# Performance work log

Measured on AMD Instinct MI355X. Metric: run time of the kernel, lower is better.

## Reference

```python
import jax, jax.numpy as jnp
import numpy as np

N = 16384      # tokens
D_IN = 256     # input feature dim
D = 1024       # d_model
H = 2048       # expert hidden dim (2 * d_model)
E = 8          # n_experts
K = 2          # top_k
OUT = 2        # output classes
EPS = 1e-5


def layernorm(x, g, b):
    m = jnp.mean(x, axis=-1, keepdims=True)
    v = jnp.mean(jnp.square(x - m), axis=-1, keepdims=True)
    return (x - m) * jax.lax.rsqrt(v + EPS) * g + b


def setup_inputs() -> dict:
    key = jax.random.key(0)
    ks = jax.random.split(key, 10)
    s_in = 1.0 / np.sqrt(D_IN)
    s_d = 1.0 / np.sqrt(D)
    s_h = 1.0 / np.sqrt(H)
    return {
        "x": jax.random.normal(ks[0], (N, D_IN), jnp.float32),
        "w_in": jax.random.normal(ks[1], (D_IN, D), jnp.float32) * s_in,
        "b_in": jnp.zeros((D,), jnp.float32),
        "g_in": jnp.ones((D,), jnp.float32),
        "beta_in": jnp.zeros((D,), jnp.float32),
        "w_gate": jax.random.normal(ks[2], (D, E), jnp.float32) * s_d,
        "w1": jax.random.normal(ks[3], (E, D, H), jnp.float32) * s_d,
        "b1": jnp.zeros((E, H), jnp.float32),
        "w2": jax.random.normal(ks[4], (E, H, D), jnp.float32) * s_h,
        "b2": jnp.zeros((E, D), jnp.float32),
        "g_moe": jnp.ones((D,), jnp.float32),
        "beta_moe": jnp.zeros((D,), jnp.float32),
        "g_out": jnp.ones((D,), jnp.float32),
        "beta_out": jnp.zeros((D,), jnp.float32),
        "w_cls": jax.random.normal(ks[5], (D, OUT), jnp.float32) * s_d,
        "b_cls": jnp.zeros((OUT,), jnp.float32),
    }


def reference(x, w_in, b_in, g_in, beta_in, w_gate, w1, b1, w2, b2,
              g_moe, beta_moe, g_out, beta_out, w_cls, b_cls):
    # input projection + norm
    h = layernorm(x @ w_in + b_in, g_in, beta_in)            # [N, D]
    # router: softmax then top-k, renormalize over selected experts
    probs = jax.nn.softmax(h @ w_gate, axis=-1)              # [N, E]
    _, top_idx = jax.lax.top_k(probs, K)                     # [N, K]
    sel = jax.nn.one_hot(top_idx, E, dtype=probs.dtype).sum(axis=1)  # [N, E] 0/1
    gates = probs * sel
    gates = gates / (jnp.sum(gates, axis=-1, keepdims=True) + 1e-9)
    # experts: weighted combine; gate==0 tokens contribute nothing (same math
    # as the torch masked gather/scatter-add, dropout off in eval)
    mixed = jnp.zeros_like(h)
    for e in range(E):  # fixed, small expert count
        expert_out = jax.nn.gelu(h @ w1[e] + b1[e]) @ w2[e] + b2[e]  # [N, D]
        mixed = mixed + gates[:, e:e + 1] * expert_out
    out = layernorm(h + mixed, g_moe, beta_moe)
    out = layernorm(out, g_out, beta_out)
    return out @ w_cls + b_cls                               # [N, OUT]
```

## Files before the change

kernel.cpp:

```cpp
#include <hip/hip_runtime.h>
#include <hip/hip_bf16.h>

#define D_IN 256
#define DM   1024
#define HD   2048
#define NE   8
#define NTOK 16384

typedef __attribute__((ext_vector_type(8))) short short8;
typedef __attribute__((ext_vector_type(4))) float f32x4;
typedef unsigned int uint;

#define MT_TOFF1 0
#define MT_TOFF2 512
#define MT_CNT1  1536
#define MT_P1    1600
#define MT_OFF1  1664
#define MT_CNT2  1728
#define MT_PCNT2 1856
#define MT_TOTAL 1984

__device__ inline ushort f2bf(float v){
  __hip_bfloat16 b = __float2bfloat16(v);
  return *reinterpret_cast<ushort*>(&b);
}
__device__ inline float bf2f(ushort u){
  __hip_bfloat16 b = *reinterpret_cast<__hip_bfloat16*>(&u);
  return __bfloat162float(b);
}

__device__ inline float gelu_fast(float x){
  float u = 0.7978845608028654f * x * (1.0f + 0.044715f*x*x);
  return x / (1.0f + __expf(-2.0f*u));
}

__device__ inline void gload16(const void* g, void* l){
  __builtin_amdgcn_global_load_lds(
      (const __attribute__((address_space(1))) void*)g,
      (__attribute__((address_space(3))) void*)l, 16, 0, 0);
}


__global__ __launch_bounds__(256) void transpose_both_kernel(
    const float* __restrict__ w1, const float* __restrict__ w2,
    ushort* __restrict__ w1t, ushort* __restrict__ w2t)
{
  __shared__ float tile[32][33];
  int bid = blockIdx.x;
  int which = bid >> 14;
  int r = bid & 16383;
  const float* src; ushort* dst; int R, C;
  if (which==0){ src=w1; dst=w1t; R=DM; C=HD; }
  else         { src=w2; dst=w2t; R=HD; C=DM; }
  int nbx = C/32, nby = R/32;
  int e = r / (nbx*nby); int rem = r % (nbx*nby);
  int c0 = (rem % nbx)*32, r0 = (rem / nbx)*32;
  src += (size_t)e*R*C; dst += (size_t)e*R*C;
  int tx = threadIdx.x & 31, ty = threadIdx.x >> 5;
  #pragma unroll
  for (int rr = ty; rr < 32; rr += 8)
    tile[rr][tx] = src[(size_t)(r0+rr)*C + c0+tx];
  __syncthreads();
  #pragma unroll
  for (int rr = ty; rr < 32; rr += 8)
    dst[(size_t)(c0+rr)*R + r0+tx] = f2bf(tile[tx][rr]);
}

__global__ __launch_bounds__(256) void split_x_kernel(
    const float* __restrict__ x, ushort* __restrict__ xs3)
{
  int g = blockIdx.x*256 + threadIdx.x;
  int e0 = g*4;
  int row = e0 >> 8, col = e0 & 255;
  f32x4 v = *(const f32x4*)(x + (size_t)row*D_IN + col);
  ushort4 hi, mi, lo;
  #pragma unroll
  for (int i=0;i<4;++i){
    float f = v[i];
    ushort h = f2bf(f);       float fh = bf2f(h);
    ushort m = f2bf(f - fh);  float fm = bf2f(m);
    ushort l = f2bf(f - fh - fm);
    ((ushort*)&hi)[i]=h; ((ushort*)&mi)[i]=m; ((ushort*)&lo)[i]=l;
  }
  ushort* base = xs3 + (size_t)row*768 + col;
  *(ushort4*)(base)       = hi;
  *(ushort4*)(base + 256) = mi;
  *(ushort4*)(base + 512) = lo;
}

__global__ __launch_bounds__(256) void transpose_split3_kernel(
    const float* __restrict__ src, ushort* __restrict__ dst)
{
  __shared__ float tile[32][33];
  int c0 = blockIdx.x*32, r0 = blockIdx.y*32;
  int tx = threadIdx.x & 31, ty = threadIdx.x >> 5;
  #pragma unroll
  for (int rr = ty; rr < 32; rr += 8)
    tile[rr][tx] = src[(size_t)(r0+rr)*DM + c0+tx];
  __syncthreads();
  #pragma unroll
  for (int rr = ty; rr < 32; rr += 8){
    float f = tile[tx][rr];
    ushort h = f2bf(f);       float fh = bf2f(h);
    ushort m = f2bf(f - fh);  float fm = bf2f(m);
    ushort l = f2bf(f - fh - fm);
    ushort* d = dst + (size_t)(c0+rr)*768 + r0 + tx;
    d[0]   = h;
    d[256] = m;
    d[512] = l;
  }
}

__global__ __launch_bounds__(256) void wgate_t_kernel(
    const float* __restrict__ w_gate, float* __restrict__ wgt)
{
  int e = blockIdx.x;
  for (int j = threadIdx.x; j < DM; j += 256)
    wgt[(size_t)e*DM + j] = w_gate[(size_t)j*NE + e];
}

__global__ __launch_bounds__(256) void gemm_router(
    const ushort* __restrict__ A,
    const ushort* __restrict__ BT,
    const float* __restrict__ b_in,
    float* __restrict__ y)
{
  __shared__ ushort As[3][128*32];
  __shared__ ushort Bs[3][128*32];
  const int tid = threadIdx.x;
  const int w = tid>>6, l = tid&63;
  const int wm = w>>1, wn = w&1;
  const int bm0 = blockIdx.y*128, bn0 = blockIdx.x*128;
  const int lr = l&15, lk = l>>4;
  const int rsub = l>>2;
  const int csub = ((l&3) ^ ((l>>3)&3)) * 8;

  const ushort* ag[2]; const ushort* bg[2];
  int aslot[2];
  #pragma unroll
  for (int i=0;i<2;++i){
    int ra = bm0 + w*32 + i*16 + rsub;
    int rb = bn0 + w*32 + i*16 + rsub;
    ag[i] = A  + (size_t)ra*768 + csub;
    bg[i] = BT + (size_t)rb*768 + csub;
    aslot[i] = (w*32 + i*16)*32;
  }

  const int pOffT[6] = {0,256,0,256,512,0};
  const int qOffT[6] = {0,0,256,256,0,512};
  auto stage = [&](int db, int t){
    int pOff = pOffT[t>>3] + (t&7)*32;
    int qOff = qOffT[t>>3] + (t&7)*32;
    #pragma unroll
    for (int i=0;i<2;++i){
      gload16(ag[i]+pOff, (ushort*)As[db] + aslot[i]);
      gload16(bg[i]+qOff, (ushort*)Bs[db] + aslot[i]);
    }
  };

  f32x4 acc[4][4] = {};
  const int NK = 48;
  stage(0, 0); stage(1, 1);
  int cur = 0;
  for (int t=0; t<NK; ++t){
    int sb = cur - 1; if (sb < 0) sb = 2;
    if (t+2 < NK)     { stage(sb, t+2); asm volatile("s_waitcnt vmcnt(8)" ::: "memory"); }
    else if (t+1 < NK){                 asm volatile("s_waitcnt vmcnt(4)" ::: "memory"); }
    else              {                 asm volatile("s_waitcnt vmcnt(0)" ::: "memory"); }
    __builtin_amdgcn_s_barrier();
    short8 af[4], bf[4];
    #pragma unroll
    for (int i=0;i<4;++i)
      af[i] = *(const short8*)(As[cur] + (wm*64 + i*16 + lr)*32 + (lk ^ ((lr>>1)&3))*8);
    #pragma unroll
    for (int j=0;j<4;++j)
      bf[j] = *(const short8*)(Bs[cur] + (wn*64 + j*16 + lr)*32 + (lk ^ ((lr>>1)&3))*8);
    __builtin_amdgcn_s_setprio(1);
    #pragma unroll
    for (int i=0;i<4;++i){
      #pragma unroll
      for (int j=0;j<4;++j)
        acc[i][j] = __builtin_amdgcn_mfma_f32_16x16x32_bf16(af[i], bf[j], acc[i][j], 0, 0, 0);
    }
    __builtin_amdgcn_s_setprio(0);
    __builtin_amdgcn_s_barrier();
    cur = cur + 1; if (cur > 2) cur = 0;
  }

  #pragma unroll
  for (int i=0;i<4;++i){
    #pragma unroll
    for (int j=0;j<4;++j){
      int n = bn0 + wn*64 + j*16 + lr;
      float bn_ = b_in[n];
      #pragma unroll
      for (int r=0;r<4;++r){
        int m = bm0 + wm*64 + i*16 + lk*4 + r;
        y[(size_t)m*DM + n] = acc[i][j][r] + bn_;
      }
    }
  }
}

__device__ inline double wredd(double v){
  #pragma unroll
  for (int o=32;o>0;o>>=1) v += __shfl_xor(v, o, 64);
  return v;
}

__global__ __launch_bounds__(256) void ln_router_kernel(
    const float* __restrict__ g_in, const float* __restrict__ beta_in,
    const float* __restrict__ wgt,
    ushort* __restrict__ hbf, float* __restrict__ resid,
    float* __restrict__ gates, int* __restrict__ selmask)
{
  int tok = blockIdx.x*4 + (threadIdx.x>>6);
  int l = threadIdx.x & 63;
  float* row = resid + (size_t)tok*DM;
  float u[16];
  double s=0.0, q=0.0;
  #pragma unroll
  for (int r=0;r<16;++r){ u[r]=row[l+64*r]; s+=u[r]; q+=(double)u[r]*u[r]; }
  s = wredd(s); q = wredd(q);
  double mean = s*(1.0/1024.0);
  double var  = q*(1.0/1024.0) - mean*mean;
  double rstd = 1.0/sqrt(var + 1e-5);

  double lg[NE];
  #pragma unroll
  for (int e=0;e<NE;++e) lg[e]=0.0;
  float hv[16];
  #pragma unroll
  for (int r=0;r<16;++r){
    int j = l + 64*r;
    double v = ((double)u[r]-mean)*rstd*(double)g_in[j] + (double)beta_in[j];
    hv[r] = (float)v;
    #pragma unroll
    for (int e=0;e<NE;++e) lg[e] += v*(double)wgt[(size_t)e*DM + j];
  }
  #pragma unroll
  for (int r=0;r<16;++r){
    int j = l + 64*r;
    row[j] = hv[r];
    hbf[(size_t)tok*DM + j] = f2bf(hv[r]);
  }
  #pragma unroll
  for (int e=0;e<NE;++e) lg[e] = wredd(lg[e]);

  if (l==0){
    double mx = lg[0];
    #pragma unroll
    for (int e=1;e<NE;++e) mx = lg[e]>mx ? lg[e] : mx;
    double p[NE]; double sum=0.0;
    #pragma unroll
    for (int e=0;e<NE;++e){ p[e]=exp(lg[e]-mx); sum+=p[e]; }
    #pragma unroll
    for (int e=0;e<NE;++e) p[e]/=sum;
    int i1=0;
    for (int e=1;e<NE;++e) if (p[e]>p[i1]) i1=e;
    int i2=-1;
    for (int e=0;e<NE;++e){ if (e==i1) continue; if (i2<0 || p[e]>p[i2]) i2=e; }
    double denom = p[i1]+p[i2]+1e-9;
    float g[NE];
    #pragma unroll
    for (int e=0;e<NE;++e) g[e]=0.f;
    g[i1]=(float)(p[i1]/denom);
    g[i2]=(float)(p[i2]/denom);
    #pragma unroll
    for (int e=0;e<NE;++e) gates[(size_t)tok*NE+e]=g[e];
    selmask[tok] = (1<<i1)|(1<<i2);
  }
}

__global__ __launch_bounds__(256) void builder_count(
    const int* __restrict__ selmask, uint* __restrict__ bc1, uint* __restrict__ bc2)
{
  __shared__ uint c1[8], c2s[16];
  int b = blockIdx.x, tid = threadIdx.x;
  if (tid<8) c1[tid]=0;
  if (tid<16) c2s[tid]=0;
  __syncthreads();
  int m = selmask[b*256+tid];
  int ea = __ffs(m)-1, eb = 31-__clz(m);
  atomicAdd(&c1[ea],1u); atomicAdd(&c1[eb],1u);
  atomicAdd(&c2s[ea],1u); atomicAdd(&c2s[8+eb],1u);
  __syncthreads();
  if (tid<8) bc1[b*8+tid]=c1[tid];
  if (tid<16) bc2[b*16+tid]=c2s[tid];
}

__global__ __launch_bounds__(256) void builder_scan(
    const uint* __restrict__ bc1, const uint* __restrict__ bc2,
    uint* __restrict__ meta, int nch, int TPC)
{
  int tid = threadIdx.x;
  int c = tid/24, k = tid%24;
  if (c < nch){
    if (k < 8){
      uint run=0;
      for (int b=c*TPC; b<(c+1)*TPC; ++b){ meta[MT_TOFF1 + b*8 + k] = run; run += bc1[b*8+k]; }
      meta[MT_CNT1 + c*8 + k] = run;
    } else {
      int k2 = k-8;
      uint run=0;
      for (int b=c*TPC; b<(c+1)*TPC; ++b){ meta[MT_TOFF2 + b*16 + k2] = run; run += bc2[b*16+k2]; }
      meta[MT_CNT2 + c*16 + k2] = run;
      meta[MT_PCNT2 + c*16 + k2] = ((run + 127u)/128u)*128u;
    }
  }
  __syncthreads();
  if (tid < nch){
    uint off=0;
    for (int e=0;e<8;++e){
      uint cn = meta[MT_CNT1 + tid*8 + e];
      uint p = ((cn+127u)/128u)*128u;
      meta[MT_P1 + tid*8 + e] = p;
      meta[MT_OFF1 + tid*8 + e] = off;
      off += p;
    }
  }
}

__device__ inline int exclscan256(int v, int* sc, int tid){
  sc[tid]=v; __syncthreads();
  #pragma unroll
  for (int o=1;o<256;o<<=1){
    int x = (tid>=o) ? sc[tid-o] : 0;
    __syncthreads();
    sc[tid]+=x;
    __syncthreads();
  }
  int incl = sc[tid]; __syncthreads();
  return incl - v;
}

__global__ __launch_bounds__(256) void builder_fill(
    const int* __restrict__ selmask, const uint* __restrict__ meta,
    int* __restrict__ ids1, int CH)
{
  __shared__ int sc[256];
  int b = blockIdx.x, tid = threadIdx.x;
  int t = b*256 + tid;
  int c = t / CH;
  int m = selmask[t];
  int ea = __ffs(m)-1, eb = 31-__clz(m);
  int ja=0, jb=0;
  for (int e=0;e<8;++e){
    int r0 = exclscan256((ea==e)?1:0, sc, tid);
    if (ea==e) ja = r0;
    int r1 = exclscan256((eb==e)?1:0, sc, tid);
    if (eb==e) jb = r1;
  }
  {
    uint j    = meta[MT_TOFF2 + b*16 + ea] + (uint)ja;
    ids1[(c*8+ea)*CH + j] = t;
  }
  {
    uint j    = meta[MT_TOFF2 + b*16 + 8 + eb] + (uint)jb;
    uint pos1 = meta[MT_CNT2 + c*16 + eb] + j;
    ids1[(c*8+eb)*CH + pos1] = t;
  }
}

__global__ __launch_bounds__(256) void gemm_ffn1(
    const ushort* __restrict__ Abase,
    const ushort* __restrict__ BT,
    const int*   __restrict__ rows,
    const uint*  __restrict__ pcnt,
    const uint*  __restrict__ off1,
    const float* __restrict__ bias,
    ushort* __restrict__ t1,
    int K, int N, int CH)
{
  const int e = blockIdx.z;
  const int bm0 = blockIdx.y*128;
  if ((uint)bm0 >= pcnt[e]) return;
  const int bn0 = blockIdx.x*128;

  __shared__ ushort As[3][128*32];
  __shared__ ushort Bs[3][128*32];
  const int tid = threadIdx.x;
  const int w = tid>>6, l = tid&63;
  const int wm = w>>1, wn = w&1;
  const int lr = l&15, lk = l>>4;
  const int rsub = l>>2;
  const int csub = ((l&3) ^ ((l>>3)&3)) * 8;

  const ushort* ag[2]; const ushort* bg[2];
  int slot[2];
  #pragma unroll
  for (int i=0;i<2;++i){
    int ra = w*32 + i*16 + rsub;
    int id = rows[e*CH + bm0 + ra];
    ag[i] = Abase + (size_t)id*K + csub;
    int rb = bn0 + w*32 + i*16 + rsub;
    bg[i] = BT + (size_t)e*N*K + (size_t)rb*K + csub;
    slot[i] = (w*32 + i*16)*32;
  }

  auto stage = [&](int db, int kt){
    #pragma unroll
    for (int i=0;i<2;++i){
      gload16(ag[i]+kt, (ushort*)As[db] + slot[i]);
      gload16(bg[i]+kt, (ushort*)Bs[db] + slot[i]);
    }
  };

  f32x4 acc[4][4] = {};
  const int NK = K>>5;
  stage(0, 0); stage(1, 32);
  int cur = 0;
  for (int t=0; t<NK; ++t){
    int sb = cur - 1; if (sb < 0) sb = 2;
    if (t+2 < NK)     { stage(sb, (t+2)<<5); asm volatile("s_waitcnt vmcnt(8)" ::: "memory"); }
    else if (t+1 < NK){                      asm volatile("s_waitcnt vmcnt(4)" ::: "memory"); }
    else              {                      asm volatile("s_waitcnt vmcnt(0)" ::: "memory"); }
    __builtin_amdgcn_s_barrier();
    short8 af[4], bf[4];
    #pragma unroll
    for (int i=0;i<4;++i)
      af[i] = *(const short8*)(As[cur] + (wm*64 + i*16 + lr)*32 + (lk ^ ((lr>>1)&3))*8);
    #pragma unroll
    for (int j=0;j<4;++j)
      bf[j] = *(const short8*)(Bs[cur] + (wn*64 + j*16 + lr)*32 + (lk ^ ((lr>>1)&3))*8);
    __builtin_amdgcn_s_setprio(1);
    #pragma unroll
    for (int i=0;i<4;++i){
      #pragma unroll
      for (int j=0;j<4;++j)
        acc[i][j] = __builtin_amdgcn_mfma_f32_16x16x32_bf16(af[i], bf[j], acc[i][j], 0, 0, 0);
    }
    __builtin_amdgcn_s_setprio(0);
    __builtin_amdgcn_s_barrier();
    cur = cur + 1; if (cur > 2) cur = 0;
  }

  #pragma unroll
  for (int i=0;i<4;++i){
    #pragma unroll
    for (int j=0;j<4;++j){
      int n = bn0 + wn*64 + j*16 + lr;
      float bn_ = bias[(size_t)e*N + n];
      #pragma unroll
      for (int r=0;r<4;++r){
        int mloc = wm*64 + i*16 + lk*4 + r;
        float v = acc[i][j][r] + bn_;
        size_t trow = (size_t)off1[e] + bm0 + mloc;
        t1[trow*N + n] = f2bf(gelu_fast(v));
      }
    }
  }
}

__global__ __launch_bounds__(256) void gemm_ffn2(
    const ushort* __restrict__ t1,
    const ushort* __restrict__ BT,
    const int*   __restrict__ ids1,
    const uint*  __restrict__ cnt1,
    const uint*  __restrict__ pcnt1,
    const uint*  __restrict__ off1,
    const float* __restrict__ bias,
    const float* __restrict__ gates,
    float* __restrict__ resid,
    int K, int N, int CH)
{
  const int e = blockIdx.z;
  const int bm0 = blockIdx.y*128;
  if ((uint)bm0 >= pcnt1[e]) return;
  const uint scnt = cnt1[e];
  const int bn0 = blockIdx.x*128;

  __shared__ ushort As[3][128*32];
  __shared__ ushort Bs[3][128*32];
  const int tid = threadIdx.x;
  const int w = tid>>6, l = tid&63;
  const int wm = w>>1, wn = w&1;
  const int lr = l&15, lk = l>>4;
  const int rsub = l>>2;
  const int csub = ((l&3) ^ ((l>>3)&3)) * 8;

  const ushort* ag[2]; const ushort* bg[2];
  int slot[2];
  #pragma unroll
  for (int i=0;i<2;++i){
    int ra = w*32 + i*16 + rsub;
    size_t arow = (size_t)off1[e] + bm0 + ra;
    ag[i] = t1 + arow*K + csub;
    int rb = bn0 + w*32 + i*16 + rsub;
    bg[i] = BT + (size_t)e*N*K + (size_t)rb*K + csub;
    slot[i] = (w*32 + i*16)*32;
  }

  auto stage = [&](int db, int kt){
    #pragma unroll
    for (int i=0;i<2;++i){
      gload16(ag[i]+kt, (ushort*)As[db] + slot[i]);
      gload16(bg[i]+kt, (ushort*)Bs[db] + slot[i]);
    }
  };

  f32x4 acc[4][4] = {};
  const int NK = K>>5;
  stage(0, 0); stage(1, 32);
  int cur = 0;
  for (int t=0; t<NK; ++t){
    int sb = cur - 1; if (sb < 0) sb = 2;
    if (t+2 < NK)     { stage(sb, (t+2)<<5); asm volatile("s_waitcnt vmcnt(8)" ::: "memory"); }
    else if (t+1 < NK){                      asm volatile("s_waitcnt vmcnt(4)" ::: "memory"); }
    else              {                      asm volatile("s_waitcnt vmcnt(0)" ::: "memory"); }
    __builtin_amdgcn_s_barrier();
    short8 af[4], bf[4];
    #pragma unroll
    for (int i=0;i<4;++i)
      af[i] = *(const short8*)(As[cur] + (wm*64 + i*16 + lr)*32 + (lk ^ ((lr>>1)&3))*8);
    #pragma unroll
    for (int j=0;j<4;++j)
      bf[j] = *(const short8*)(Bs[cur] + (wn*64 + j*16 + lr)*32 + (lk ^ ((lr>>1)&3))*8);
    __builtin_amdgcn_s_setprio(1);
    #pragma unroll
    for (int i=0;i<4;++i){
      #pragma unroll
      for (int j=0;j<4;++j)
        acc[i][j] = __builtin_amdgcn_mfma_f32_16x16x32_bf16(af[i], bf[j], acc[i][j], 0, 0, 0);
    }
    __builtin_amdgcn_s_setprio(0);
    __builtin_amdgcn_s_barrier();
    cur = cur + 1; if (cur > 2) cur = 0;
  }

  #pragma unroll
  for (int i=0;i<4;++i){
    #pragma unroll
    for (int j=0;j<4;++j){
      int n = bn0 + wn*64 + j*16 + lr;
      float bn_ = bias[(size_t)e*N + n];
      #pragma unroll
      for (int r=0;r<4;++r){
        int mloc = wm*64 + i*16 + lk*4 + r;
        int mg = bm0 + mloc;
        if ((uint)mg < scnt){
          int tok = ids1[e*CH + mg];
          float g = gates[(size_t)tok*NE + e];
          atomicAdd(&resid[(size_t)tok*N + n], g*(acc[i][j][r] + bn_));
        }
      }
    }
  }
}

__global__ __launch_bounds__(256) void final_kernel(
    const float* __restrict__ resid,
    const float* __restrict__ g_moe, const float* __restrict__ beta_moe,
    const float* __restrict__ g_out, const float* __restrict__ beta_out,
    const float* __restrict__ w_cls, const float* __restrict__ b_cls,
    float* __restrict__ out)
{
  int tok = blockIdx.x*4 + (threadIdx.x>>6);
  int l = threadIdx.x & 63;
  const float* row = resid + (size_t)tok*DM;
  float u[16];
  double s=0.0,q=0.0;
  #pragma unroll
  for (int r=0;r<16;++r){ u[r]=row[l + 64*r]; s+=u[r]; q+=(double)u[r]*u[r]; }
  s=wredd(s); q=wredd(q);
  double m1 = s*(1.0/1024.0), v1 = q*(1.0/1024.0)-m1*m1;
  double rs1 = 1.0/sqrt(v1+1e-5);
  float tv[16]; double s2=0.0,q2=0.0;
  #pragma unroll
  for (int r=0;r<16;++r){
    int j = l+64*r;
    float vv = (float)((u[r]-m1)*rs1)*g_moe[j] + beta_moe[j];
    tv[r]=vv; s2+=vv; q2+=(double)vv*vv;
  }
  s2=wredd(s2); q2=wredd(q2);
  double m2=s2*(1.0/1024.0), v2=q2*(1.0/1024.0)-m2*m2;
  double rs2=1.0/sqrt(v2+1e-5);
  double p0=0.0,p1=0.0;
  #pragma unroll
  for (int r=0;r<16;++r){
    int j=l+64*r;
    double y=((double)tv[r]-m2)*rs2*(double)g_out[j]+(double)beta_out[j];
    p0+=y*(double)w_cls[j*2]; p1+=y*(double)w_cls[j*2+1];
  }
  p0=wredd(p0); p1=wredd(p1);
  if (l==0){
    out[(size_t)tok*2  ]=(float)(p0+(double)b_cls[0]);
    out[(size_t)tok*2+1]=(float)(p1+(double)b_cls[1]);
  }
}

extern "C" void kernel_launch(void* const* d_in, const int* in_sizes, int n_in,
                              void* d_out, int out_size, void* d_ws, size_t ws_size,
                              hipStream_t stream)
{
  (void)in_sizes; (void)n_in; (void)out_size;
  const float* x       = (const float*)d_in[0];
  const float* w_in    = (const float*)d_in[1];
  const float* b_in    = (const float*)d_in[2];
  const float* g_in    = (const float*)d_in[3];
  const float* beta_in = (const float*)d_in[4];
  const float* w_gate  = (const float*)d_in[5];
  const float* w1      = (const float*)d_in[6];
  const float* b1      = (const float*)d_in[7];
  const float* w2      = (const float*)d_in[8];
  const float* b2      = (const float*)d_in[9];
  const float* g_moe   = (const float*)d_in[10];
  const float* beta_mo = (const float*)d_in[11];
  const float* g_out   = (const float*)d_in[12];
  const float* beta_ou = (const float*)d_in[13];
  const float* w_cls   = (const float*)d_in[14];
  const float* b_cls   = (const float*)d_in[15];
  float* out = (float*)d_out;

  char* p = (char*)d_ws;
  ushort* w1t   = (ushort*)p; p += (size_t)NE*HD*DM*2;
  ushort* w2t   = (ushort*)p; p += (size_t)NE*DM*HD*2;
  ushort* hbf   = (ushort*)p; p += (size_t)NTOK*DM*2;
  float*  resid = (float*)p;  p += (size_t)NTOK*DM*4;
  float*  gates = (float*)p;  p += (size_t)NTOK*NE*4;
  int*    selmk = (int*)p;    p += (size_t)NTOK*4;
  int*    ids1  = (int*)p;    p += (size_t)NE*NTOK*4;
  ushort* wt3   = (ushort*)p; p += (size_t)DM*768*2;
  float*  wgt   = (float*)p;  p += (size_t)NE*DM*4;
  uint*   bc1   = (uint*)p;   p += (size_t)64*8*4;
  uint*   bc2   = (uint*)p;   p += (size_t)64*16*4;
  uint*   meta  = (uint*)p;   p += (size_t)MT_TOTAL*4;
  size_t fixed = (size_t)(p - (char*)d_ws);

  const size_t xs3_bytes = (size_t)NTOK*768*2;
  size_t t1b1 = ((size_t)2*NTOK        + 2048)*HD*2;
  size_t t1b2 = ((size_t)2*(NTOK/2)    + 2048)*HD*2;
  size_t t1b4 = ((size_t)2*(NTOK/4)    + 2048)*HD*2;
  int nch = 8;
  if      (ws_size >= fixed + (t1b1 > xs3_bytes ? t1b1 : xs3_bytes)) nch = 1;
  else if (ws_size >= fixed + (t1b2 > xs3_bytes ? t1b2 : xs3_bytes)) nch = 2;
  else if (ws_size >= fixed + (t1b4 > xs3_bytes ? t1b4 : xs3_bytes)) nch = 4;
  const int CH  = NTOK/nch;
  const int TPC = CH/256;
  ushort* t1  = (ushort*)p;
  ushort* xs3 = (ushort*)p;

  split_x_kernel<<<dim3(NTOK*D_IN/4/256), 256, 0, stream>>>(x, xs3);
  transpose_split3_kernel<<<dim3(DM/32, D_IN/32), 256, 0, stream>>>(w_in, wt3);
  wgate_t_kernel<<<dim3(NE), 256, 0, stream>>>(w_gate, wgt);
  transpose_both_kernel<<<dim3(32768), 256, 0, stream>>>(w1, w2, w1t, w2t);

  gemm_router<<<dim3(DM/128, NTOK/128), 256, 0, stream>>>(xs3, wt3, b_in, resid);
  ln_router_kernel<<<dim3(NTOK/4), 256, 0, stream>>>(g_in, beta_in, wgt,
                                                     hbf, resid, gates, selmk);

  hipMemsetAsync(ids1, 0, (size_t)NE*NTOK*4, stream);

  builder_count<<<dim3(NTOK/256), 256, 0, stream>>>(selmk, bc1, bc2);
  builder_scan<<<dim3(1), 256, 0, stream>>>(bc1, bc2, meta, nch, TPC);
  builder_fill<<<dim3(NTOK/256), 256, 0, stream>>>(selmk, meta, ids1, CH);

  for (int c = 0; c < nch; ++c) {
    gemm_ffn1<<<dim3(HD/128, CH/128, NE), 256, 0, stream>>>(
        hbf, w1t, ids1 + (size_t)c*8*CH,
        meta+MT_P1+c*8, meta+MT_OFF1+c*8, b1, t1, DM, HD, CH);
    gemm_ffn2<<<dim3(DM/128, CH/128, NE), 256, 0, stream>>>(
        t1, w2t, ids1 + (size_t)c*8*CH,
        meta+MT_CNT1+c*8, meta+MT_P1+c*8, meta+MT_OFF1+c*8,
        b2, gates, resid, HD, DM, CH);
  }

  final_kernel<<<dim3(NTOK/4), 256, 0, stream>>>(resid, g_moe, beta_mo, g_out, beta_ou,
                                                 w_cls, b_cls, out);
}
```

Baseline: 891.1 us.

## Replace atomic scatter-add of expert outputs with bf16 per-slot buffer and gather combine

```diff
diff --git a/kernel.cpp b/kernel.cpp
--- a/kernel.cpp
+++ b/kernel.cpp
@@ -211,12 +211,13 @@
 __global__ __launch_bounds__(256) void ln_router_kernel(
     const float* __restrict__ g_in, const float* __restrict__ beta_in,
     const float* __restrict__ wgt,
-    ushort* __restrict__ hbf, float* __restrict__ resid,
+    const float* __restrict__ y,
+    ushort* __restrict__ hbf,
     float* __restrict__ gates, int* __restrict__ selmask)
 {
   int tok = blockIdx.x*4 + (threadIdx.x>>6);
   int l = threadIdx.x & 63;
-  float* row = resid + (size_t)tok*DM;
+  const float* row = y + (size_t)tok*DM;
   float u[16];
   double s=0.0, q=0.0;
   #pragma unroll
@@ -241,7 +242,6 @@
   #pragma unroll
   for (int r=0;r<16;++r){
     int j = l + 64*r;
-    row[j] = hv[r];
     hbf[(size_t)tok*DM + j] = f2bf(hv[r]);
   }
   #pragma unroll
@@ -336,7 +336,7 @@
 
 __global__ __launch_bounds__(256) void builder_fill(
     const int* __restrict__ selmask, const uint* __restrict__ meta,
-    int* __restrict__ ids1, int CH)
+    int* __restrict__ ids1, int* __restrict__ rowmap, int CH, int EOC)
 {
   __shared__ int sc[256];
   int b = blockIdx.x, tid = threadIdx.x;
@@ -352,13 +352,15 @@
     if (eb==e) jb = r1;
   }
   {
-    uint j    = meta[MT_TOFF2 + b*16 + ea] + (uint)ja;
+    uint j   = meta[MT_TOFF2 + b*16 + ea] + (uint)ja;
     ids1[(c*8+ea)*CH + j] = t;
+    rowmap[2*t+0] = c*EOC + (int)meta[MT_OFF1 + c*8 + ea] + (int)j;
   }
   {
     uint j    = meta[MT_TOFF2 + b*16 + 8 + eb] + (uint)jb;
     uint pos1 = meta[MT_CNT2 + c*16 + eb] + j;
     ids1[(c*8+eb)*CH + pos1] = t;
+    rowmap[2*t+1] = c*EOC + (int)meta[MT_OFF1 + c*8 + eb] + (int)pos1;
   }
 }
 
@@ -461,7 +463,8 @@
     const uint*  __restrict__ off1,
     const float* __restrict__ bias,
     const float* __restrict__ gates,
-    float* __restrict__ resid,
+    ushort* __restrict__ eo,
+    int cbase,
     int K, int N, int CH)
 {
   const int e = blockIdx.z;
@@ -541,7 +544,8 @@
         if ((uint)mg < scnt){
           int tok = ids1[e*CH + mg];
           float g = gates[(size_t)tok*NE + e];
-          atomicAdd(&resid[(size_t)tok*N + n], g*(acc[i][j][r] + bn_));
+          size_t erow = (size_t)cbase + off1[e] + mg;
+          eo[erow*N + n] = f2bf(g*(acc[i][j][r] + bn_));
         }
       }
     }
@@ -549,7 +553,9 @@
 }
 
 __global__ __launch_bounds__(256) void final_kernel(
-    const float* __restrict__ resid,
+    const ushort* __restrict__ hbf,
+    const ushort* __restrict__ eo,
+    const int* __restrict__ rowmap,
     const float* __restrict__ g_moe, const float* __restrict__ beta_moe,
     const float* __restrict__ g_out, const float* __restrict__ beta_out,
     const float* __restrict__ w_cls, const float* __restrict__ b_cls,
@@ -557,11 +563,17 @@
 {
   int tok = blockIdx.x*4 + (threadIdx.x>>6);
   int l = threadIdx.x & 63;
-  const float* row = resid + (size_t)tok*DM;
+  const ushort* hr  = hbf + (size_t)tok*DM;
+  const ushort* er0 = eo + (size_t)rowmap[2*tok  ]*DM;
+  const ushort* er1 = eo + (size_t)rowmap[2*tok+1]*DM;
   float u[16];
   double s=0.0,q=0.0;
   #pragma unroll
-  for (int r=0;r<16;++r){ u[r]=row[l + 64*r]; s+=u[r]; q+=(double)u[r]*u[r]; }
+  for (int r=0;r<16;++r){
+    int j = l + 64*r;
+    float v = bf2f(hr[j]) + bf2f(er0[j]) + bf2f(er1[j]);
+    u[r]=v; s+=v; q+=(double)v*v;
+  }
   s=wredd(s); q=wredd(q);
   double m1 = s*(1.0/1024.0), v1 = q*(1.0/1024.0)-m1*m1;
   double rs1 = 1.0/sqrt(v1+1e-5);
@@ -579,8 +591,8 @@
   #pragma unroll
   for (int r=0;r<16;++r){
     int j=l+64*r;
-    double y=((double)tv[r]-m2)*rs2*(double)g_out[j]+(double)beta_out[j];
-    p0+=y*(double)w_cls[j*2]; p1+=y*(double)w_cls[j*2+1];
+    double yv=((double)tv[r]-m2)*rs2*(double)g_out[j]+(double)beta_out[j];
+    p0+=yv*(double)w_cls[j*2]; p1+=yv*(double)w_cls[j*2+1];
   }
   p0=wredd(p0); p1=wredd(p1);
   if (l==0){
@@ -616,27 +628,38 @@
   ushort* w1t   = (ushort*)p; p += (size_t)NE*HD*DM*2;
   ushort* w2t   = (ushort*)p; p += (size_t)NE*DM*HD*2;
   ushort* hbf   = (ushort*)p; p += (size_t)NTOK*DM*2;
-  float*  resid = (float*)p;  p += (size_t)NTOK*DM*4;
   float*  gates = (float*)p;  p += (size_t)NTOK*NE*4;
   int*    selmk = (int*)p;    p += (size_t)NTOK*4;
   int*    ids1  = (int*)p;    p += (size_t)NE*NTOK*4;
+  int*    rowmp = (int*)p;    p += (size_t)2*NTOK*4;
   ushort* wt3   = (ushort*)p; p += (size_t)DM*768*2;
   float*  wgt   = (float*)p;  p += (size_t)NE*DM*4;
   uint*   bc1   = (uint*)p;   p += (size_t)64*8*4;
   uint*   bc2   = (uint*)p;   p += (size_t)64*16*4;
   uint*   meta  = (uint*)p;   p += (size_t)MT_TOTAL*4;
-  size_t fixed = (size_t)(p - (char*)d_ws);
-
+  size_t base = (size_t)(p - (char*)d_ws);
+
+  const size_t y_bytes   = (size_t)NTOK*DM*4;
   const size_t xs3_bytes = (size_t)NTOK*768*2;
-  size_t t1b1 = ((size_t)2*NTOK        + 2048)*HD*2;
-  size_t t1b2 = ((size_t)2*(NTOK/2)    + 2048)*HD*2;
-  size_t t1b4 = ((size_t)2*(NTOK/4)    + 2048)*HD*2;
   int nch = 8;
-  if      (ws_size >= fixed + (t1b1 > xs3_bytes ? t1b1 : xs3_bytes)) nch = 1;
-  else if (ws_size >= fixed + (t1b2 > xs3_bytes ? t1b2 : xs3_bytes)) nch = 2;
-  else if (ws_size >= fixed + (t1b4 > xs3_bytes ? t1b4 : xs3_bytes)) nch = 4;
+  size_t yeo_bytes = 0, t1_bytes = 0;
+  for (int cand = 1; cand <= 8; cand <<= 1){
+    size_t eo_b = ((size_t)2*NTOK + 1024*(size_t)cand) * DM * 2;
+    size_t ye   = eo_b > y_bytes ? eo_b : y_bytes;
+    size_t t1b  = ((size_t)2*(NTOK/cand) + 2048) * HD * 2;
+    size_t tail = t1b > xs3_bytes ? t1b : xs3_bytes;
+    if (ws_size >= base + ye + tail){ nch = cand; yeo_bytes = ye; t1_bytes = t1b; break; }
+  }
+  if (yeo_bytes == 0){
+    nch = 8;
+    size_t eo_b = ((size_t)2*NTOK + 1024*8) * DM * 2;
+    yeo_bytes = eo_b > y_bytes ? eo_b : y_bytes;
+  }
   const int CH  = NTOK/nch;
   const int TPC = CH/256;
+  const int EOC = 2*CH + 1024;
+  float*  y   = (float*)p;
+  ushort* eo  = (ushort*)p;  p += yeo_bytes;
   ushort* t1  = (ushort*)p;
   ushort* xs3 = (ushort*)p;
 
@@ -645,15 +668,15 @@
   wgate_t_kernel<<<dim3(NE), 256, 0, stream>>>(w_gate, wgt);
   transpose_both_kernel<<<dim3(32768), 256, 0, stream>>>(w1, w2, w1t, w2t);
 
-  gemm_router<<<dim3(DM/128, NTOK/128), 256, 0, stream>>>(xs3, wt3, b_in, resid);
-  ln_router_kernel<<<dim3(NTOK/4), 256, 0, stream>>>(g_in, beta_in, wgt,
-                                                     hbf, resid, gates, selmk);
+  gemm_router<<<dim3(DM/128, NTOK/128), 256, 0, stream>>>(xs3, wt3, b_in, y);
+  ln_router_kernel<<<dim3(NTOK/4), 256, 0, stream>>>(g_in, beta_in, wgt, y,
+                                                     hbf, gates, selmk);
 
   hipMemsetAsync(ids1, 0, (size_t)NE*NTOK*4, stream);
 
   builder_count<<<dim3(NTOK/256), 256, 0, stream>>>(selmk, bc1, bc2);
   builder_scan<<<dim3(1), 256, 0, stream>>>(bc1, bc2, meta, nch, TPC);
-  builder_fill<<<dim3(NTOK/256), 256, 0, stream>>>(selmk, meta, ids1, CH);
+  builder_fill<<<dim3(NTOK/256), 256, 0, stream>>>(selmk, meta, ids1, rowmp, CH, EOC);
 
   for (int c = 0; c < nch; ++c) {
     gemm_ffn1<<<dim3(HD/128, CH/128, NE), 256, 0, stream>>>(
@@ -662,9 +685,10 @@
     gemm_ffn2<<<dim3(DM/128, CH/128, NE), 256, 0, stream>>>(
         t1, w2t, ids1 + (size_t)c*8*CH,
         meta+MT_CNT1+c*8, meta+MT_P1+c*8, meta+MT_OFF1+c*8,
-        b2, gates, resid, HD, DM, CH);
-  }
-
-  final_kernel<<<dim3(NTOK/4), 256, 0, stream>>>(resid, g_moe, beta_mo, g_out, beta_ou,
+        b2, gates, eo, c*EOC, HD, DM, CH);
+  }
+
+  final_kernel<<<dim3(NTOK/4), 256, 0, stream>>>(hbf, eo, rowmp,
+                                                 g_moe, beta_mo, g_out, beta_ou,
                                                  w_cls, b_cls, out);
 }
```

After: 806.9 us. 1.1x faster.
